# Kernel tuning notes

Measured on AMD Instinct MI355X. Metric: run time of the kernel, lower is better.

The kernel has to match this reference:

```python
import jax, jax.numpy as jnp
import numpy as np

N_NODES = 100000
N_EDGES = 1250000
D_FEAT = 64


def setup_inputs() -> dict:
    key = jax.random.key(0)
    kx, ke = jax.random.split(key)
    x = jax.random.normal(kx, (N_NODES, D_FEAT), dtype=jnp.float32)
    edge_index = jax.random.randint(ke, (2, N_EDGES), 0, N_NODES, dtype=jnp.int64)
    return {"x": x, "edge_index": edge_index}


def _aggregate(x, src, dst, num_nodes):
    # out[i] = sum_{e: dst[e]==i} x[src[e]]  (identity message, 'add' aggr)
    return jax.ops.segment_sum(x[src], dst, num_segments=num_nodes)


def reference(x, edge_index):
    num_nodes = x.shape[0]
    src, dst = edge_index[0], edge_index[1]  # PyG source_to_target flow
    h = _aggregate(x, src, dst, num_nodes)   # conv1
    h = jax.nn.relu(h)
    h = _aggregate(h, src, dst, num_nodes)   # conv2
    return h
```

## Files before the change

kernel.cpp:

```cpp
#include <hip/hip_runtime.h>
#include <hip/hip_bf16.h>


#define N_FEAT    64
#define BIN_SHIFT 7
#define BIN_NODES 128
#define CAPBIN    2048
#define NB_H      784
#define NSCAN     1024
#define GSTRIDE   16
#define TILE      4096
#define NPTR      (BIN_NODES + 1)

typedef unsigned int u32;
typedef unsigned short u16;
typedef __attribute__((ext_vector_type(8))) unsigned short u16x8;
typedef __attribute__((ext_vector_type(4))) unsigned int u32x4;
typedef __attribute__((ext_vector_type(2))) float f32x2;

__device__ inline u16 f2bf(float f) {
    u32 u = __builtin_bit_cast(u32, f);
    return (u16)((u + 0x7FFFu + ((u >> 16) & 1u)) >> 16);
}

__global__ __launch_bounds__(256) void partition_convert_kernel(
    const float* __restrict__ xf, u16* __restrict__ xb, int n_elems,
    const int* __restrict__ src, const int* __restrict__ dst,
    u32* __restrict__ gcur,
    u32* __restrict__ cbdata,
    int n_edges, int n_bins, int part_blocks)
{
    __shared__ u32 hist[NSCAN];
    __shared__ u32 starts[NSCAN];
    __shared__ u32 lpos[NSCAN];
    __shared__ u32 wcur[NB_H];
    __shared__ u32 sortbuf[TILE];
    __shared__ u16 binid[TILE];
    __shared__ u32 wsum[4];

    const int tid = threadIdx.x;

    if ((int)blockIdx.x >= part_blocks) {
        int i = (((int)blockIdx.x - part_blocks) * 256 + tid) * 8;
        if (i < n_elems) {
            float4 a = *(const float4*)(xf + i);
            float4 b = *(const float4*)(xf + i + 4);
            u16x8 r;
            r[0]=f2bf(a.x); r[1]=f2bf(a.y); r[2]=f2bf(a.z); r[3]=f2bf(a.w);
            r[4]=f2bf(b.x); r[5]=f2bf(b.y); r[6]=f2bf(b.z); r[7]=f2bf(b.w);
            *(u16x8*)(xb + i) = r;
        }
        return;
    }

    const int tbase = (int)blockIdx.x * TILE;
    const int tend  = min(tbase + TILE, n_edges);

    for (int i = tid; i < NSCAN; i += 256) { hist[i] = 0; lpos[i] = 0; }
    __syncthreads();

    for (int e = tbase + tid; e < tend; e += 256)
        atomicAdd(&hist[(u32)dst[e] >> BIN_SHIFT], 1u);
    __syncthreads();

    {
        const int b0 = tid * 4;
        u32 h0 = hist[b0], h1 = hist[b0+1], h2 = hist[b0+2], h3 = hist[b0+3];
        u32 s  = h0 + h1 + h2 + h3;
        u32 inc = s;
        #pragma unroll
        for (int d = 1; d < 64; d <<= 1) {
            u32 o = __shfl_up(inc, d);
            if ((tid & 63) >= d) inc += o;
        }
        if ((tid & 63) == 63) wsum[tid >> 6] = inc;
        __syncthreads();
        u32 woff = 0;
        #pragma unroll
        for (int k = 0; k < 4; ++k) if (k < (tid >> 6)) woff += wsum[k];
        u32 excl = woff + inc - s;
        starts[b0]   = excl;
        starts[b0+1] = excl + h0;
        starts[b0+2] = excl + h0 + h1;
        starts[b0+3] = excl + h0 + h1 + h2;
    }
    __syncthreads();

    const int rot = (int)(((u32)blockIdx.x * 193u) % (u32)n_bins);
    for (int i = tid; i < n_bins; i += 256) {
        int b = i + rot; if (b >= n_bins) b -= n_bins;
        u32 h = hist[b];
        if (h) wcur[b] = atomicAdd(&gcur[b * GSTRIDE], h);
    }
    __syncthreads();

    for (int e = tbase + tid; e < tend; e += 256) {
        int d = dst[e];
        int s = src[e];
        u32 b   = (u32)d >> BIN_SHIFT;
        u32 pos = starts[b] + atomicAdd(&lpos[b], 1u);
        sortbuf[pos] = ((u32)(d & (BIN_NODES - 1)) << 17) | (u32)s;
        binid[pos]   = (u16)b;
    }
    __syncthreads();

    const int cnt = tend - tbase;
    for (int j = tid; j < cnt; j += 256) {
        u32 b   = binid[j];
        u32 rel = wcur[b] + ((u32)j - starts[b]);
        if (rel < CAPBIN)
            cbdata[(size_t)b * CAPBIN + rel] = sortbuf[j];
    }
}

__global__ __launch_bounds__(256) void bin_sort_kernel(
    u32* __restrict__ cbdata,
    const u32* __restrict__ gcur,
    u32* __restrict__ nodeptr,
    int n_bins)
{
    __shared__ u32 hist[BIN_NODES];
    __shared__ u32 ptrs[NPTR];
    __shared__ u32 lpos[BIN_NODES];
    __shared__ u32 sl[CAPBIN];

    const int tid = threadIdx.x;
    const int bin = blockIdx.x;
    if (bin >= n_bins) return;

    if (tid < BIN_NODES) { hist[tid] = 0; lpos[tid] = 0; }
    __syncthreads();

    int cnt = (int)gcur[bin * GSTRIDE];
    if (cnt > CAPBIN) cnt = CAPBIN;
    u32* bd = cbdata + (size_t)bin * CAPBIN;

    for (int j = tid; j < cnt; j += 256)
        atomicAdd(&hist[bd[j] >> 17], 1u);
    __syncthreads();

    if (tid < 64) {
        u32 a = hist[2 * tid], b = hist[2 * tid + 1];
        u32 s = a + b;
        #pragma unroll
        for (int d = 1; d < 64; d <<= 1) {
            u32 o = __shfl_up(s, d);
            if (tid >= d) s += o;
        }
        ptrs[2 * tid]     = s - a - b;
        ptrs[2 * tid + 1] = s - b;
        if (tid == 63) ptrs[BIN_NODES] = s;
    }
    __syncthreads();

    for (int j = tid; j < cnt; j += 256) {
        u32 p   = bd[j];
        u32 nid = p >> 17;
        u32 pos = ptrs[nid] + atomicAdd(&lpos[nid], 1u);
        sl[pos] = p & 0x1FFFFu;
    }
    __syncthreads();

    const u32 base = (u32)bin * CAPBIN;
    for (int j = tid; j < cnt; j += 256)
        bd[j] = sl[j];
    if (tid < NPTR)
        nodeptr[(size_t)bin * NPTR + tid] = base + ptrs[tid];
}

__global__ __launch_bounds__(256) void aggregate_kernel(
    const u16* __restrict__ xin,
    const u32* __restrict__ csorted,
    const u32* __restrict__ nodeptr,
    u16* __restrict__ out_bf,
    float* __restrict__ out_f,
    int n_nodes, int pass)
{
    const int tid  = threadIdx.x;
    const int B    = blockIdx.x >> 1;
    const int half = blockIdx.x & 1;

    const int w    = tid >> 6;
    const int lane = tid & 63;
    const int grp  = lane >> 3;
    const int sub  = lane & 7;
    const char* xc = (const char*)xin;

    const int nl   = w * 8 + grp;
    const int node = B * 64 + half * 32 + nl;

    const int bin = node >> BIN_SHIFT;
    const int nid = node & (BIN_NODES - 1);
    const int s0  = (int)nodeptr[(size_t)bin * NPTR + nid];
    const int s1  = (int)nodeptr[(size_t)bin * NPTR + nid + 1];

    f32x2 a0={0.f,0.f}, a1={0.f,0.f}, a2={0.f,0.f}, a3={0.f,0.f};

    for (int jb = s0; jb < s1; jb += 8) {
        u32 myid = 0;
        if (jb + sub < s1) myid = csorted[jb + sub];
        const int m = min(8, s1 - jb);
        #pragma unroll 1
        for (int k = 0; k < m; ++k) {
            u32 s = (u32)__shfl((int)myid, (lane & 56) + k, 64);
            u32x4 v = *(const u32x4*)(xc + ((size_t)s << 7) + (sub << 4));
            a0 += (f32x2){ __builtin_bit_cast(float, v[0] << 16),
                           __builtin_bit_cast(float, v[0] & 0xFFFF0000u) };
            a1 += (f32x2){ __builtin_bit_cast(float, v[1] << 16),
                           __builtin_bit_cast(float, v[1] & 0xFFFF0000u) };
            a2 += (f32x2){ __builtin_bit_cast(float, v[2] << 16),
                           __builtin_bit_cast(float, v[2] & 0xFFFF0000u) };
            a3 += (f32x2){ __builtin_bit_cast(float, v[3] << 16),
                           __builtin_bit_cast(float, v[3] & 0xFFFF0000u) };
        }
    }

    if (node < n_nodes) {
        if (pass == 0) {
            u16x8 o;
            o[0]=f2bf(fmaxf(a0.x,0.f)); o[1]=f2bf(fmaxf(a0.y,0.f));
            o[2]=f2bf(fmaxf(a1.x,0.f)); o[3]=f2bf(fmaxf(a1.y,0.f));
            o[4]=f2bf(fmaxf(a2.x,0.f)); o[5]=f2bf(fmaxf(a2.y,0.f));
            o[6]=f2bf(fmaxf(a3.x,0.f)); o[7]=f2bf(fmaxf(a3.y,0.f));
            *(u16x8*)(out_bf + (size_t)node * N_FEAT + sub * 8) = o;
        } else {
            float* dp = out_f + (size_t)node * N_FEAT + sub * 8;
            *(float4*)dp       = (float4){a0.x, a0.y, a1.x, a1.y};
            *(float4*)(dp + 4) = (float4){a2.x, a2.y, a3.x, a3.y};
        }
    }
}

extern "C" void kernel_launch(void* const* d_in, const int* in_sizes, int n_in,
                              void* d_out, int out_size, void* d_ws, size_t ws_size,
                              hipStream_t stream) {
    const float* x          = (const float*)d_in[0];
    const int*   edge_index = (const int*)d_in[1];

    const int n_edges = in_sizes[1] / 2;
    const int* src = edge_index;
    const int* dst = edge_index + n_edges;

    const int n_nodes = out_size / N_FEAT;
    const int n_bins  = (n_nodes + BIN_NODES - 1) >> BIN_SHIFT;
    float* out = (float*)d_out;

    const size_t xb_bytes    = (size_t)out_size * sizeof(u16);
    const size_t hb_bytes    = (size_t)out_size * sizeof(u16);
    const size_t cb_bytes    = (size_t)n_bins * CAPBIN * sizeof(u32);
    const size_t np_bytes    = (size_t)n_bins * NPTR * sizeof(u32);
    const size_t gcur_bytes  = (size_t)NB_H * GSTRIDE * sizeof(u32);

    char* w = (char*)d_ws;
    u16* xb      = (u16*)w;              w += xb_bytes;
    u16* hb      = (u16*)w;              w += hb_bytes;
    u32* cbdata  = (u32*)w;              w += cb_bytes;
    u32* nodeptr = (u32*)w;              w += np_bytes;
    u32* gcur    = (u32*)w;

    hipMemsetAsync(gcur, 0, gcur_bytes, stream);

    const int part_blocks = (n_edges + TILE - 1) / TILE;
    const int conv_blocks = (out_size / 8 + 255) / 256;
    partition_convert_kernel<<<part_blocks + conv_blocks, 256, 0, stream>>>(
        x, xb, out_size, src, dst, gcur, cbdata, n_edges, n_bins, part_blocks);

    bin_sort_kernel<<<n_bins, 256, 0, stream>>>(cbdata, gcur, nodeptr, n_bins);

    const int agg_blocks = 2 * ((n_nodes + 63) / 64);
    aggregate_kernel<<<agg_blocks, 256, 0, stream>>>(xb, cbdata, nodeptr, hb, nullptr, n_nodes, 0);
    aggregate_kernel<<<agg_blocks, 256, 0, stream>>>(hb, cbdata, nodeptr, nullptr, out, n_nodes, 1);
}
```

Baseline: 170.2 us.

## Degree-sort nodes within each bin to balance aggregation wave workloads

The bin sort kernel now also runs a counting sort of each bin's 128 nodes by in-degree (capped at 63) and writes the resulting permutation to a new nodemap buffer. The aggregation kernels then assign nodes to 8-lane groups in that degree-sorted order, so groups within a wavefront have similar edge counts. This targets divergence, where a whole wave waits on its highest-degree node. The cost is extra shared-memory atomics and scans in the sort kernel, one more indirect load per node, and output writes that land in a permuted order within each bin.

```diff
diff --git a/kernel.cpp b/kernel.cpp
--- a/kernel.cpp
+++ b/kernel.cpp
@@ -117,18 +117,23 @@
     u32* __restrict__ cbdata,
     const u32* __restrict__ gcur,
     u32* __restrict__ nodeptr,
+    u32* __restrict__ nodemap,
     int n_bins)
 {
     __shared__ u32 hist[BIN_NODES];
     __shared__ u32 ptrs[NPTR];
     __shared__ u32 lpos[BIN_NODES];
     __shared__ u32 sl[CAPBIN];
+    __shared__ u32 dh[64];
+    __shared__ u32 dptr[64];
+    __shared__ u32 dpos[64];
 
     const int tid = threadIdx.x;
     const int bin = blockIdx.x;
     if (bin >= n_bins) return;
 
     if (tid < BIN_NODES) { hist[tid] = 0; lpos[tid] = 0; }
+    if (tid < 64) { dh[tid] = 0; dpos[tid] = 0; }
     __syncthreads();
 
     int cnt = (int)gcur[bin * GSTRIDE];
@@ -151,7 +156,27 @@
         ptrs[2 * tid + 1] = s - b;
         if (tid == 63) ptrs[BIN_NODES] = s;
     }
-    __syncthreads();
+    if (tid < BIN_NODES)
+        atomicAdd(&dh[min(hist[tid], 63u)], 1u);
+    __syncthreads();
+
+    if (tid < 64) {
+        u32 v = dh[tid];
+        u32 s = v;
+        #pragma unroll
+        for (int d = 1; d < 64; d <<= 1) {
+            u32 o = __shfl_up(s, d);
+            if (tid >= d) s += o;
+        }
+        dptr[tid] = s - v;
+    }
+    __syncthreads();
+
+    if (tid < BIN_NODES) {
+        u32 key  = min(hist[tid], 63u);
+        u32 rank = dptr[key] + atomicAdd(&dpos[key], 1u);
+        nodemap[(size_t)bin * BIN_NODES + rank] = (u32)tid;
+    }
 
     for (int j = tid; j < cnt; j += 256) {
         u32 p   = bd[j];
@@ -172,13 +197,12 @@
     const u16* __restrict__ xin,
     const u32* __restrict__ csorted,
     const u32* __restrict__ nodeptr,
+    const u32* __restrict__ nodemap,
     u16* __restrict__ out_bf,
     float* __restrict__ out_f,
     int n_nodes, int pass)
 {
     const int tid  = threadIdx.x;
-    const int B    = blockIdx.x >> 1;
-    const int half = blockIdx.x & 1;
 
     const int w    = tid >> 6;
     const int lane = tid & 63;
@@ -187,10 +211,12 @@
     const char* xc = (const char*)xin;
 
     const int nl   = w * 8 + grp;
-    const int node = B * 64 + half * 32 + nl;
-
-    const int bin = node >> BIN_SHIFT;
-    const int nid = node & (BIN_NODES - 1);
+    const int rg   = (int)blockIdx.x * 32 + nl;
+    const int bin  = rg >> BIN_SHIFT;
+    const int rank = rg & (BIN_NODES - 1);
+    const int nid  = (int)nodemap[(size_t)bin * BIN_NODES + rank];
+    const int node = bin * BIN_NODES + nid;
+
     const int s0  = (int)nodeptr[(size_t)bin * NPTR + nid];
     const int s1  = (int)nodeptr[(size_t)bin * NPTR + nid + 1];
 
@@ -249,6 +275,7 @@
     const size_t hb_bytes    = (size_t)out_size * sizeof(u16);
     const size_t cb_bytes    = (size_t)n_bins * CAPBIN * sizeof(u32);
     const size_t np_bytes    = (size_t)n_bins * NPTR * sizeof(u32);
+    const size_t nm_bytes    = (size_t)n_bins * BIN_NODES * sizeof(u32);
     const size_t gcur_bytes  = (size_t)NB_H * GSTRIDE * sizeof(u32);
 
     char* w = (char*)d_ws;
@@ -256,6 +283,7 @@
     u16* hb      = (u16*)w;              w += hb_bytes;
     u32* cbdata  = (u32*)w;              w += cb_bytes;
     u32* nodeptr = (u32*)w;              w += np_bytes;
+    u32* nodemap = (u32*)w;              w += nm_bytes;
     u32* gcur    = (u32*)w;
 
     hipMemsetAsync(gcur, 0, gcur_bytes, stream);
@@ -265,9 +293,9 @@
     partition_convert_kernel<<<part_blocks + conv_blocks, 256, 0, stream>>>(
         x, xb, out_size, src, dst, gcur, cbdata, n_edges, n_bins, part_blocks);
 
-    bin_sort_kernel<<<n_bins, 256, 0, stream>>>(cbdata, gcur, nodeptr, n_bins);
-
-    const int agg_blocks = 2 * ((n_nodes + 63) / 64);
-    aggregate_kernel<<<agg_blocks, 256, 0, stream>>>(xb, cbdata, nodeptr, hb, nullptr, n_nodes, 0);
-    aggregate_kernel<<<agg_blocks, 256, 0, stream>>>(hb, cbdata, nodeptr, nullptr, out, n_nodes, 1);
-}
+    bin_sort_kernel<<<n_bins, 256, 0, stream>>>(cbdata, gcur, nodeptr, nodemap, n_bins);
+
+    const int agg_blocks = (n_bins * BIN_NODES) / 32;
+    aggregate_kernel<<<agg_blocks, 256, 0, stream>>>(xb, cbdata, nodeptr, nodemap, hb, nullptr, n_nodes, 0);
+    aggregate_kernel<<<agg_blocks, 256, 0, stream>>>(hb, cbdata, nodeptr, nodemap, nullptr, out, n_nodes, 1);
+}
```

After: 177.6 us. 1.04x slower.
